# Kernel optimization log

Measured on AMD Instinct MI355X. Metric: run time of the kernel, lower is better.

Reference implementation:

```python
import jax, jax.numpy as jnp
import numpy as np

N_NODES = 100000
N_EDGES = 800000
FEATURE_DIM = 128
DEPTH = 3


def setup_inputs() -> dict:
    key = jax.random.key(0)
    k1, k2, k3 = jax.random.split(key, 3)
    x = jax.random.normal(k1, (N_NODES, FEATURE_DIM), dtype=jnp.float32)
    edge_index = jax.random.randint(k2, (2, N_EDGES), 0, N_NODES, dtype=jnp.int32)
    W = jax.random.normal(k3, (FEATURE_DIM, FEATURE_DIM), dtype=jnp.float32) * (1.0 / np.sqrt(FEATURE_DIM))
    b = jnp.zeros((FEATURE_DIM,), dtype=jnp.float32)
    return {"x": x, "edge_index": edge_index, "W": W, "b": b}


def reference(x, edge_index, W, b):
    n = x.shape[0]
    # PyG GCNConv default: add self-loops, symmetric normalization
    loop = jnp.arange(n, dtype=edge_index.dtype)
    src = jnp.concatenate([edge_index[0], loop])  # [E+N]
    dst = jnp.concatenate([edge_index[1], loop])  # [E+N]
    ones = jnp.ones(src.shape[0], dtype=x.dtype)
    deg = jax.ops.segment_sum(ones, dst, num_segments=n)  # in-degree incl. self-loop
    dis = jnp.where(deg > 0, jax.lax.rsqrt(deg), 0.0)  # deg^{-1/2}
    norm = (dis[src] * dis[dst])[:, None]  # [E+N, 1]

    # depth iterations share the SAME conv weights (time-invariant)
    for _ in range(DEPTH):
        h = x @ W  # [N, D] linear transform first (PyG order)
        msg = h[src] * norm  # gather + normalize, [E+N, D]
        agg = jax.ops.segment_sum(msg, dst, num_segments=n)  # scatter-add
        x = jax.nn.relu(agg + b)  # bias, NullControl adds 0, dropout_rate=0 is identity
    return x
```

## Files before the change

kernel.cpp:

```cpp
#include <hip/hip_runtime.h>

#define FD 128
#define CAP 64

typedef __attribute__((ext_vector_type(8))) short short8;
typedef __attribute__((ext_vector_type(4))) float floatx4;

__device__ inline unsigned short f2bf(float f) {
  unsigned u = __float_as_uint(f);
  u += 0x7fffu + ((u >> 16) & 1u);
  return (unsigned short)(u >> 16);
}
__device__ inline float lo16f(unsigned v) { return __uint_as_float(v << 16); }
__device__ inline float hi16f(unsigned v) { return __uint_as_float(v & 0xffff0000u); }
__device__ inline int imin(int a, int b) { return a < b ? a : b; }
__device__ inline unsigned umin(unsigned a, unsigned b) { return a < b ? a : b; }

__global__ __launch_bounds__(256) void k_prep(const float* __restrict__ W,
                                              short* __restrict__ whi,
                                              int* __restrict__ cursor, int N,
                                              int zB) {
  int b = blockIdx.x;
  if (b < zB) {
    int i = b * 256 + threadIdx.x;
    if (i < N) cursor[i] = 0;
  } else {
    int idx = (b - zB) * 256 + threadIdx.x;
    int j = idx & 7, lane = (idx >> 3) & 63, kt = (idx >> 9) & 3, ct = idx >> 11;
    int k = kt * 32 + (lane >> 4) * 8 + j;
    int n = ct * 16 + (lane & 15);
    whi[idx] = (short)f2bf(W[k * FD + n]);
  }
}

__global__ __launch_bounds__(256) void k_fill(const int* __restrict__ src,
                                              const int* __restrict__ dst,
                                              int* __restrict__ cursor,
                                              int* __restrict__ buck, int E) {
  int slice = blockIdx.x & 7;
  int e = (blockIdx.x >> 3) * 256 + threadIdx.x;
  if (e < E) {
    int d = dst[e];
    if (((d >> 4) & 7) == slice) {
      int s = src[e];
      int pos = atomicAdd(&cursor[d], 1);
      if (pos < CAP) buck[(size_t)d * CAP + pos] = s;
    }
  }
}

template <bool ABF16>
__global__ __launch_bounds__(256) void k_gemm(const void* __restrict__ Av,
                                              const short* __restrict__ Wf_hi,
                                              const int* __restrict__ cursor,
                                              unsigned short* __restrict__ H, int N) {
  __shared__ short whi[FD * FD];
  int tid = threadIdx.x;
#pragma unroll
  for (int it = 0; it < 8; ++it) {
    int idx = (it * 256 + tid) * 8;
    *(short8*)&whi[idx] = *(const short8*)&Wf_hi[idx];
  }
  __syncthreads();

  int wid = tid >> 6, lane = tid & 63;
  int quad = lane >> 4, m = lane & 15;
  int rbase = blockIdx.x * 128 + wid * 32;

  short8 ahi[2][4];
#pragma unroll
  for (int t = 0; t < 2; ++t) {
    int arow = rbase + t * 16 + m;
    if (arow >= N) arow = N - 1;
    if (ABF16) {
      const unsigned short* ap = (const unsigned short*)Av + (size_t)arow * FD;
#pragma unroll
      for (int kt = 0; kt < 4; ++kt)
        ahi[t][kt] = *(const short8*)(ap + kt * 32 + quad * 8);
    } else {
      const float* ap = (const float*)Av + (size_t)arow * FD;
#pragma unroll
      for (int kt = 0; kt < 4; ++kt) {
        const float* p = ap + kt * 32 + quad * 8;
        float4 a0 = *(const float4*)p;
        float4 a1 = *(const float4*)(p + 4);
        ahi[t][kt][0] = (short)f2bf(a0.x); ahi[t][kt][1] = (short)f2bf(a0.y);
        ahi[t][kt][2] = (short)f2bf(a0.z); ahi[t][kt][3] = (short)f2bf(a0.w);
        ahi[t][kt][4] = (short)f2bf(a1.x); ahi[t][kt][5] = (short)f2bf(a1.y);
        ahi[t][kt][6] = (short)f2bf(a1.z); ahi[t][kt][7] = (short)f2bf(a1.w);
      }
    }
  }

  float dis0[4], dis1[4];
#pragma unroll
  for (int r = 0; r < 4; ++r) {
    int row0 = imin(rbase + quad * 4 + r, N - 1);
    int row1 = imin(rbase + 16 + quad * 4 + r, N - 1);
    dis0[r] = rsqrtf((float)(imin(cursor[row0], CAP) + 1));
    dis1[r] = rsqrtf((float)(imin(cursor[row1], CAP) + 1));
  }

#pragma unroll
  for (int ct = 0; ct < 8; ++ct) {
    floatx4 acc0 = {0.f, 0.f, 0.f, 0.f}, acc1 = {0.f, 0.f, 0.f, 0.f};
#pragma unroll
    for (int kt = 0; kt < 4; ++kt) {
      int fo = (((ct << 2) + kt) * 64 + lane) * 8;
      short8 bhi = *(const short8*)&whi[fo];
      acc0 = __builtin_amdgcn_mfma_f32_16x16x32_bf16(ahi[0][kt], bhi, acc0, 0, 0, 0);
      acc1 = __builtin_amdgcn_mfma_f32_16x16x32_bf16(ahi[1][kt], bhi, acc1, 0, 0, 0);
    }
#pragma unroll
    for (int r = 0; r < 4; ++r) {
      int row0 = rbase + quad * 4 + r;
      int row1 = rbase + 16 + quad * 4 + r;
      if (row0 < N) H[(size_t)row0 * FD + ct * 16 + m] = f2bf(acc0[r] * dis0[r]);
      if (row1 < N) H[(size_t)row1 * FD + ct * 16 + m] = f2bf(acc1[r] * dis1[r]);
    }
  }
}

template <bool OUTBF16>
__global__ __launch_bounds__(256) void k_agg(const unsigned int* __restrict__ h,
                                             const int* __restrict__ cursor,
                                             const int* __restrict__ buck,
                                             const float* __restrict__ bias,
                                             void* __restrict__ out, int N) {
  int wid = __builtin_amdgcn_readfirstlane(threadIdx.x >> 6);
  int lane = threadIdx.x & 63;
  int i = blockIdx.x * 4 + wid;
  if (i >= N) return;
  int deg = imin(cursor[i], CAP);
  float disi = rsqrtf((float)(deg + 1));
  unsigned v = h[(size_t)i * 64 + lane];
  float a0 = lo16f(v), a1 = hi16f(v);
  float b0 = 0.f, b1 = 0.f, c0 = 0.f, c1 = 0.f, d0 = 0.f, d1 = 0.f;

  const int4* bp = (const int4*)(buck + (size_t)i * CAP);
  int niter = (deg + 7) >> 3;
  for (int it = 0; it < niter; ++it) {
    int4 sa = bp[2 * it];
    int4 sb = bp[2 * it + 1];
    int srcs[8] = {sa.x, sa.y, sa.z, sa.w, sb.x, sb.y, sb.z, sb.w};
    unsigned g[8];
#pragma unroll
    for (int j = 0; j < 8; ++j) {
      unsigned su = (unsigned)__builtin_amdgcn_readfirstlane(srcs[j]);
      su = umin(su, (unsigned)(N - 1));
      g[j] = h[(size_t)su * 64 + lane];
    }
    int done = it * 8;
#pragma unroll
    for (int j = 0; j < 8; ++j) {
      float w = (done + j < deg) ? 1.f : 0.f;
      float l = lo16f(g[j]), hh = hi16f(g[j]);
      if (j == 0 || j == 4) { a0 = fmaf(w, l, a0); a1 = fmaf(w, hh, a1); }
      else if (j == 1 || j == 5) { b0 = fmaf(w, l, b0); b1 = fmaf(w, hh, b1); }
      else if (j == 2 || j == 6) { c0 = fmaf(w, l, c0); c1 = fmaf(w, hh, c1); }
      else { d0 = fmaf(w, l, d0); d1 = fmaf(w, hh, d1); }
    }
  }

  float2 bb = ((const float2*)bias)[lane];
  float o0 = fmaxf(fmaf(disi, (a0 + b0) + (c0 + d0), bb.x), 0.f);
  float o1 = fmaxf(fmaf(disi, (a1 + b1) + (c1 + d1), bb.y), 0.f);
  if (OUTBF16) {
    unsigned pk = ((unsigned)f2bf(o1) << 16) | (unsigned)f2bf(o0);
    ((unsigned*)out)[(size_t)i * 64 + lane] = pk;
  } else {
    ((float2*)out)[(size_t)i * 64 + lane] = make_float2(o0, o1);
  }
}


extern "C" void kernel_launch(void* const* d_in, const int* in_sizes, int n_in,
                              void* d_out, int out_size, void* d_ws, size_t ws_size,
                              hipStream_t stream) {
  const float* x = (const float*)d_in[0];
  const int* ei = (const int*)d_in[1];
  const float* Wg = (const float*)d_in[2];
  const float* b = (const float*)d_in[3];
  int N = in_sizes[0] / FD;
  int E = in_sizes[1] / 2;
  const int* src = ei;
  const int* dst = ei + E;

  char* p = (char*)d_ws;
  auto alloc = [&](size_t bytes) {
    void* r = (void*)p;
    p += (bytes + 255) & ~(size_t)255;
    return r;
  };
  int* cursor = (int*)alloc((size_t)N * 4);
  int* buck = (int*)alloc((size_t)N * CAP * 4);
  unsigned short* h = (unsigned short*)alloc((size_t)N * FD * 2);
  unsigned short* xb = (unsigned short*)alloc((size_t)N * FD * 2);
  short* wf_hi = (short*)alloc((size_t)FD * FD * 2);

  int zB = (N + 255) / 256;
  int wB = FD * FD / 256;
  int gG = (N + 127) / 128;
  int gA = (N + 3) / 4;
  int gE = (E + 255) / 256;

  k_prep<<<zB + wB, 256, 0, stream>>>(Wg, wf_hi, cursor, N, zB);
  k_fill<<<8 * gE, 256, 0, stream>>>(src, dst, cursor, buck, E);

  k_gemm<false><<<gG, 256, 0, stream>>>(x, wf_hi, cursor, h, N);
  k_agg<true><<<gA, 256, 0, stream>>>((const unsigned*)h, cursor, buck, b, xb, N);
  k_gemm<true><<<gG, 256, 0, stream>>>(xb, wf_hi, cursor, h, N);
  k_agg<true><<<gA, 256, 0, stream>>>((const unsigned*)h, cursor, buck, b, xb, N);
  k_gemm<true><<<gG, 256, 0, stream>>>(xb, wf_hi, cursor, h, N);
  k_agg<false><<<gA, 256, 0, stream>>>((const unsigned*)h, cursor, buck, b, d_out, N);
}
```

Before: 294.6 us.

## Fuse all GCN phases into one persistent kernel with grid barriers

Replaces the sequence of separate launches (prep, fill, three gemm/agg pairs) with a single persistent kernel of fixed grid size that iterates over work with grid-stride loops and separates phases with an atomic-counter grid barrier. Each block converts W to bf16 directly into its shared memory, removing the staging buffer and its kernel. The intent is to remove launch gaps and tail effects between phases; it risks reduced latency hiding in the gather-heavy aggregation, barrier spin overhead, and deadlock or incorrectness if not all blocks are co-resident (the spin loop has a timeout).

```diff
diff --git a/kernel.cpp b/kernel.cpp
--- a/kernel.cpp
+++ b/kernel.cpp
@@ -2,6 +2,7 @@
 
 #define FD 128
 #define CAP 64
+#define GRID 784
 
 typedef __attribute__((ext_vector_type(8))) short short8;
 typedef __attribute__((ext_vector_type(4))) float floatx4;
@@ -16,56 +17,37 @@
 __device__ inline int imin(int a, int b) { return a < b ? a : b; }
 __device__ inline unsigned umin(unsigned a, unsigned b) { return a < b ? a : b; }
 
-__global__ __launch_bounds__(256) void k_prep(const float* __restrict__ W,
-                                              short* __restrict__ whi,
-                                              int* __restrict__ cursor, int N,
-                                              int zB) {
-  int b = blockIdx.x;
-  if (b < zB) {
-    int i = b * 256 + threadIdx.x;
-    if (i < N) cursor[i] = 0;
-  } else {
-    int idx = (b - zB) * 256 + threadIdx.x;
-    int j = idx & 7, lane = (idx >> 3) & 63, kt = (idx >> 9) & 3, ct = idx >> 11;
-    int k = kt * 32 + (lane >> 4) * 8 + j;
-    int n = ct * 16 + (lane & 15);
-    whi[idx] = (short)f2bf(W[k * FD + n]);
-  }
-}
-
-__global__ __launch_bounds__(256) void k_fill(const int* __restrict__ src,
-                                              const int* __restrict__ dst,
-                                              int* __restrict__ cursor,
-                                              int* __restrict__ buck, int E) {
-  int slice = blockIdx.x & 7;
-  int e = (blockIdx.x >> 3) * 256 + threadIdx.x;
-  if (e < E) {
-    int d = dst[e];
-    if (((d >> 4) & 7) == slice) {
-      int s = src[e];
-      int pos = atomicAdd(&cursor[d], 1);
-      if (pos < CAP) buck[(size_t)d * CAP + pos] = s;
-    }
-  }
+__device__ inline void gridbar(int* bar, int target) {
+  __syncthreads();
+  if (threadIdx.x == 0) {
+    __threadfence();
+    atomicAdd(bar, 1);
+    int spins = 0;
+    while (__hip_atomic_load(bar, __ATOMIC_RELAXED, __HIP_MEMORY_SCOPE_AGENT) <
+           target) {
+      __builtin_amdgcn_s_sleep(2);
+      if (++spins > (1 << 23)) break;
+    }
+    __threadfence();
+  }
+  __syncthreads();
+}
+
+__global__ __launch_bounds__(256) void k_init(int* __restrict__ cursor,
+                                              int* __restrict__ bar, int N) {
+  int i = blockIdx.x * 256 + threadIdx.x;
+  if (i < N) cursor[i] = 0;
+  if (i == 0) *bar = 0;
 }
 
 template <bool ABF16>
-__global__ __launch_bounds__(256) void k_gemm(const void* __restrict__ Av,
-                                              const short* __restrict__ Wf_hi,
-                                              const int* __restrict__ cursor,
-                                              unsigned short* __restrict__ H, int N) {
-  __shared__ short whi[FD * FD];
+__device__ __forceinline__ void gemm_phase(const void* Av, const short* whi,
+                                           const int* cursor,
+                                           unsigned short* H, int N, int bid) {
   int tid = threadIdx.x;
-#pragma unroll
-  for (int it = 0; it < 8; ++it) {
-    int idx = (it * 256 + tid) * 8;
-    *(short8*)&whi[idx] = *(const short8*)&Wf_hi[idx];
-  }
-  __syncthreads();
-
   int wid = tid >> 6, lane = tid & 63;
   int quad = lane >> 4, m = lane & 15;
-  int rbase = blockIdx.x * 128 + wid * 32;
+  int rbase = bid * 128 + wid * 32;
 
   short8 ahi[2][4];
 #pragma unroll
@@ -122,14 +104,12 @@
 }
 
 template <bool OUTBF16>
-__global__ __launch_bounds__(256) void k_agg(const unsigned int* __restrict__ h,
-                                             const int* __restrict__ cursor,
-                                             const int* __restrict__ buck,
-                                             const float* __restrict__ bias,
-                                             void* __restrict__ out, int N) {
+__device__ __forceinline__ void agg_phase(const unsigned* h, const int* cursor,
+                                          const int* buck, const float* bias,
+                                          void* out, int N, int vb) {
   int wid = __builtin_amdgcn_readfirstlane(threadIdx.x >> 6);
   int lane = threadIdx.x & 63;
-  int i = blockIdx.x * 4 + wid;
+  int i = vb * 4 + wid;
   if (i >= N) return;
   int deg = imin(cursor[i], CAP);
   float disi = rsqrtf((float)(deg + 1));
@@ -171,6 +151,63 @@
   } else {
     ((float2*)out)[(size_t)i * 64 + lane] = make_float2(o0, o1);
   }
+}
+
+__global__ __launch_bounds__(256, 4) void k_main(
+    const float* __restrict__ x, const int* __restrict__ src,
+    const int* __restrict__ dst, const float* __restrict__ W,
+    const float* __restrict__ bias, int* cursor, int* buck, unsigned short* h,
+    unsigned short* xb, float2* out, int* bar, int N, int E, int gE, int gG,
+    int gA) {
+  __shared__ short whi[FD * FD];
+  int tid = threadIdx.x;
+  int B = blockIdx.x;
+  int NB = gridDim.x;
+
+#pragma unroll
+  for (int it = 0; it < 64; ++it) {
+    int idx = it * 256 + tid;
+    int j = idx & 7, lane = (idx >> 3) & 63, kt = (idx >> 9) & 3, ct = idx >> 11;
+    int k = kt * 32 + (lane >> 4) * 8 + j;
+    int n = ct * 16 + (lane & 15);
+    whi[idx] = (short)f2bf(W[k * FD + n]);
+  }
+
+  {
+    int slice = B & 7;
+    for (int c = B >> 3; c < gE; c += NB >> 3) {
+      int e = c * 256 + tid;
+      if (e < E) {
+        int d = __builtin_nontemporal_load(&dst[e]);
+        if (((d >> 4) & 7) == slice) {
+          int s = __builtin_nontemporal_load(&src[e]);
+          int pos = atomicAdd(&cursor[d], 1);
+          if (pos < CAP) buck[(size_t)d * CAP + pos] = s;
+        }
+      }
+    }
+  }
+  gridbar(bar, 1 * NB);
+
+  for (int vb = B; vb < gG; vb += NB) gemm_phase<false>(x, whi, cursor, h, N, vb);
+  gridbar(bar, 2 * NB);
+
+  for (int vb = B; vb < gA; vb += NB)
+    agg_phase<true>((const unsigned*)h, cursor, buck, bias, xb, N, vb);
+  gridbar(bar, 3 * NB);
+
+  for (int vb = B; vb < gG; vb += NB) gemm_phase<true>(xb, whi, cursor, h, N, vb);
+  gridbar(bar, 4 * NB);
+
+  for (int vb = B; vb < gA; vb += NB)
+    agg_phase<true>((const unsigned*)h, cursor, buck, bias, xb, N, vb);
+  gridbar(bar, 5 * NB);
+
+  for (int vb = B; vb < gG; vb += NB) gemm_phase<true>(xb, whi, cursor, h, N, vb);
+  gridbar(bar, 6 * NB);
+
+  for (int vb = B; vb < gA; vb += NB)
+    agg_phase<false>((const unsigned*)h, cursor, buck, bias, out, N, vb);
 }
 
 
@@ -192,25 +229,19 @@
     p += (bytes + 255) & ~(size_t)255;
     return r;
   };
+  int* bar = (int*)alloc(256);
   int* cursor = (int*)alloc((size_t)N * 4);
   int* buck = (int*)alloc((size_t)N * CAP * 4);
   unsigned short* h = (unsigned short*)alloc((size_t)N * FD * 2);
   unsigned short* xb = (unsigned short*)alloc((size_t)N * FD * 2);
-  short* wf_hi = (short*)alloc((size_t)FD * FD * 2);
-
-  int zB = (N + 255) / 256;
-  int wB = FD * FD / 256;
+  float2* outp = (float2*)d_out;
+
+  int gE = (E + 255) / 256;
   int gG = (N + 127) / 128;
   int gA = (N + 3) / 4;
-  int gE = (E + 255) / 256;
-
-  k_prep<<<zB + wB, 256, 0, stream>>>(Wg, wf_hi, cursor, N, zB);
-  k_fill<<<8 * gE, 256, 0, stream>>>(src, dst, cursor, buck, E);
-
-  k_gemm<false><<<gG, 256, 0, stream>>>(x, wf_hi, cursor, h, N);
-  k_agg<true><<<gA, 256, 0, stream>>>((const unsigned*)h, cursor, buck, b, xb, N);
-  k_gemm<true><<<gG, 256, 0, stream>>>(xb, wf_hi, cursor, h, N);
-  k_agg<true><<<gA, 256, 0, stream>>>((const unsigned*)h, cursor, buck, b, xb, N);
-  k_gemm<true><<<gG, 256, 0, stream>>>(xb, wf_hi, cursor, h, N);
-  k_agg<false><<<gA, 256, 0, stream>>>((const unsigned*)h, cursor, buck, b, d_out, N);
-}
+
+  int zB = (N + 255) / 256;
+  k_init<<<zB, 256, 0, stream>>>(cursor, bar, N);
+  k_main<<<GRID, 256, 0, stream>>>(x, src, dst, Wg, b, cursor, buck, h, xb,
+                                   outp, bar, N, E, gE, gG, gA);
+}
```

New measurement: 1.116 ms. 279% more time.
